# Kernel tuning notes

Measured on AMD Instinct MI355X. Metric: run time of the kernel, lower is better.

The kernel has to match this reference:

```python
import jax, jax.numpy as jnp
import numpy as np
import math

# ---- static configuration (mirrors Renderer defaults) ----
S = 129                                 # density cube side
L = math.ceil(S * math.sqrt(3))         # padded/rotation cube side = 224
C_ABS = 0.2                             # absorption coefficient c
LIGHTS = [
    {'dir': (2, 1, 1),    'rgb': (1.0, 69.0 / 255.0, 25.0 / 255.0)},
    {'dir': (-1, 0.5, 0), 'rgb': (227.0 / 255.0, 1.0, 66.0 / 255.0)},
]


def yp_from_light(l):
    ld = np.asarray(l, dtype=np.float64)
    ld = ld / np.sqrt(np.sum(ld ** 2))
    y = -math.asin(ld[0])
    if ld[2] < 0:
        y = -math.pi - y
    y = y * 180.0 / math.pi
    p = math.asin(ld[1]) * 180.0 / math.pi
    return y, p


def rot_matrix(yaw_deg, pitch_deg, order):
    # yaw about the y (height) axis, pitch about the x axis, roll = 0
    y = math.radians(yaw_deg)
    p = math.radians(pitch_deg)
    Ry = np.array([[math.cos(y), 0.0, math.sin(y)],
                   [0.0, 1.0, 0.0],
                   [-math.sin(y), 0.0, math.cos(y)]], dtype=np.float32)
    Rp = np.array([[1.0, 0.0, 0.0],
                   [0.0, math.cos(p), -math.sin(p)],
                   [0.0, math.sin(p), math.cos(p)]], dtype=np.float32)
    return Ry @ Rp if order == 'ypr' else Rp @ Ry

# base normalized sampling grid (align_corners=True convention), (x,y,z) order
_lin = np.linspace(-1.0, 1.0, L, dtype=np.float32)
_zz, _yy, _xx = np.meshgrid(_lin, _lin, _lin, indexing='ij')
BASE_XYZ = np.stack([_xx, _yy, _zz], axis=-1)   # [L,L,L,3]


def rotate_volume(vol, R):
    """Trilinear resampling of vol [B,C,D,H,W] under rotation R (zero padding)."""
    B, Ch, D, H, W = vol.shape
    src = jnp.einsum('dhwc,kc->dhwk', jnp.asarray(BASE_XYZ), jnp.asarray(R))
    xs = (src[..., 0] + 1.0) * 0.5 * (W - 1)
    ys = (src[..., 1] + 1.0) * 0.5 * (H - 1)
    zs = (src[..., 2] + 1.0) * 0.5 * (D - 1)
    x0 = jnp.floor(xs).astype(jnp.int32)
    y0 = jnp.floor(ys).astype(jnp.int32)
    z0 = jnp.floor(zs).astype(jnp.int32)
    wx = (xs - x0).astype(vol.dtype)
    wy = (ys - y0).astype(vol.dtype)
    wz = (zs - z0).astype(vol.dtype)
    flat = vol.reshape(B, Ch, D * H * W)

    def gather(zi, yi, xi):
        inb = ((zi >= 0) & (zi < D) & (yi >= 0) & (yi < H) & (xi >= 0) & (xi < W)).astype(vol.dtype)
        idx = ((jnp.clip(zi, 0, D - 1) * H + jnp.clip(yi, 0, H - 1)) * W
               + jnp.clip(xi, 0, W - 1)).reshape(-1)
        return jnp.take(flat, idx, axis=2).reshape(B, Ch, D, H, W) * inb

    out = (gather(z0,     y0,     x0)     * ((1 - wz) * (1 - wy) * (1 - wx))
         + gather(z0,     y0,     x0 + 1) * ((1 - wz) * (1 - wy) * wx)
         + gather(z0,     y0 + 1, x0)     * ((1 - wz) * wy * (1 - wx))
         + gather(z0,     y0 + 1, x0 + 1) * ((1 - wz) * wy * wx)
         + gather(z0 + 1, y0,     x0)     * (wz * (1 - wy) * (1 - wx))
         + gather(z0 + 1, y0,     x0 + 1) * (wz * (1 - wy) * wx)
         + gather(z0 + 1, y0 + 1, x0)     * (wz * wy * (1 - wx))
         + gather(z0 + 1, y0 + 1, x0 + 1) * (wz * wy * wx))
    return out


def _revcumsum(a):
    # torch.flip(cumsum(flip(a,[2]),2),[2]) : reverse cumulative sum along depth
    return jnp.flip(jnp.cumsum(jnp.flip(a, 2), axis=2), 2)


def setup_inputs() -> dict:
    key = jax.random.key(0)
    d = jax.random.uniform(key, (1, 1, S, S, S), dtype=jnp.float32)
    return {'d': d}


def reference(d):
    bs, _, Sd, _, _ = d.shape
    i = L // 2 - Sd // 2
    j = i + Sd
    light_array = jnp.zeros((bs, 3, Sd, Sd, Sd), dtype=d.dtype)
    for l in LIGHTS:
        y, p = yp_from_light(l['dir'])
        up = jnp.zeros((bs, 1, L, L, L), dtype=d.dtype).at[:, :, i:j, i:j, i:j].set(d)
        up = rotate_volume(up, rot_matrix(y, p, 'ypr'))
        up = jnp.exp(-C_ABS * _revcumsum(up))           # transmittance toward light
        up = rotate_volume(up, rot_matrix(-y, -p, 'rpy'))
        color = jnp.asarray(l['rgb'], dtype=d.dtype).reshape(1, 3, 1, 1, 1)
        light_array = light_array + up[:, :, i:j, i:j, i:j] * color
    t = jnp.exp(-C_ABS * _revcumsum(d))                  # view-ray transmittance
    out = C_ABS * jnp.sum(d * light_array * t, axis=2)   # background = 0
    return jnp.clip(out, 0.0, 1.0)
```

## Files before the change

### kernel.cpp

```cpp
#include <hip/hip_runtime.h>
#include <hip/hip_fp16.h>
#include <math.h>

#ifndef M_PI
#define M_PI 3.14159265358979323846
#endif

#define SS   129
#define LL   224
#define LL2  (LL*LL)
#define LL3  (LL*LL*LL)
#define SS2  (SS*SS)
#define SS3  (SS*SS*SS)
#define CABS 0.2f
#define PAD  48

#define BLO 45.5f
#define BHI 178.5f

#define NT1  28
#define NTZ16 14
#define ROTG  (2 * NTZ16 * 784)
#define NT3  17
#define NBZ16 9
#define BACKG (2 * NBZ16 * 289)
#define NTZ  28

#define NSEG 16
#define SEGZ 9
#define DSEGT (NSEG * SS2)
#define PREB1 ((DSEGT + 255) / 256)
#define PRERUNB 7
#define N4   (SS3 / 4)
#define CVT4B ((N4 + 1 + 255) / 256)
#define PREG (PREB1 + PRERUNB + CVT4B)
#define SUFG (392 + PREB1)
#define TEXPB (2 * NTZ * LL2 / 256)

#define RBX 21
#define RBY 16
#define RBZ 18
#define RBN (RBX*RBY*RBZ)
#define RSXZ (RBX*RBZ)

#define BBX 21
#define BBY 16
#define BBZ 19
#define BBN (BBX*BBY*BBZ)
#define BSXZ (BBX*BBZ)

struct Mat3 { float m[9]; };
struct F3   { float x, y, z; };

__device__ __forceinline__ F3 tile_center(const Mat3& M, int ox, int oy, int oz) {
    float cbx = fmaf((float)ox + 3.5f, 2.0f / 223.0f, -1.0f);
    float cby = fmaf((float)oy + 3.5f, 2.0f / 223.0f, -1.0f);
    float cbz = fmaf((float)oz + 3.5f, 2.0f / 223.0f, -1.0f);
    F3 qc;
    qc.x = fmaf(fmaf(M.m[0], cbx, fmaf(M.m[1], cby, M.m[2] * cbz)), 111.5f, 111.5f);
    qc.y = fmaf(fmaf(M.m[3], cbx, fmaf(M.m[4], cby, M.m[5] * cbz)), 111.5f, 111.5f);
    qc.z = fmaf(fmaf(M.m[6], cbx, fmaf(M.m[7], cby, M.m[8] * cbz)), 111.5f, 111.5f);
    return qc;
}

__device__ __forceinline__ F3 tile_center16(const Mat3& M, int ox, int oy, int oz) {
    float cbx = fmaf((float)ox + 3.5f, 2.0f / 223.0f, -1.0f);
    float cby = fmaf((float)oy + 3.5f, 2.0f / 223.0f, -1.0f);
    float cbz = fmaf((float)oz + 7.5f, 2.0f / 223.0f, -1.0f);
    F3 qc;
    qc.x = fmaf(fmaf(M.m[0], cbx, fmaf(M.m[1], cby, M.m[2] * cbz)), 111.5f, 111.5f);
    qc.y = fmaf(fmaf(M.m[3], cbx, fmaf(M.m[4], cby, M.m[5] * cbz)), 111.5f, 111.5f);
    qc.z = fmaf(fmaf(M.m[6], cbx, fmaf(M.m[7], cby, M.m[8] * cbz)), 111.5f, 111.5f);
    return qc;
}

__device__ __forceinline__ bool tile_accept(F3 qc, F3 H) {
    return !(qc.x + H.x < BLO || qc.x - H.x > BHI ||
             qc.y + H.y < BLO || qc.y - H.y > BHI ||
             qc.z + H.z < BLO || qc.z - H.z > BHI);
}

__device__ __forceinline__ void qmap(const Mat3& M, int x, int y, int z,
                                     float& qx, float& qy, float& qz) {
    float bx = fmaf((float)x, 2.0f / 223.0f, -1.0f);
    float by = fmaf((float)y, 2.0f / 223.0f, -1.0f);
    float bz = fmaf((float)z, 2.0f / 223.0f, -1.0f);
    qx = fmaf(fmaf(M.m[0], bx, fmaf(M.m[1], by, M.m[2] * bz)), 111.5f, 111.5f);
    qy = fmaf(fmaf(M.m[3], bx, fmaf(M.m[4], by, M.m[5] * bz)), 111.5f, 111.5f);
    qz = fmaf(fmaf(M.m[6], bx, fmaf(M.m[7], by, M.m[8] * bz)), 111.5f, 111.5f);
}

__device__ __forceinline__ float fetch_d(const float* __restrict__ d, int z, int y, int x) {
    unsigned zz = (unsigned)(z - PAD), yy = (unsigned)(y - PAD), xx = (unsigned)(x - PAD);
    return (zz < (unsigned)SS && yy < (unsigned)SS && xx < (unsigned)SS)
        ? d[((int)zz * SS + (int)yy) * SS + (int)xx] : 0.0f;
}

__device__ __forceinline__ float fetch_d16(const __half* __restrict__ d, int z, int y, int x) {
    unsigned zz = (unsigned)(z - PAD), yy = (unsigned)(y - PAD), xx = (unsigned)(x - PAD);
    return (zz < (unsigned)SS && yy < (unsigned)SS && xx < (unsigned)SS)
        ? __half2float(d[((int)zz * SS + (int)yy) * SS + (int)xx]) : 0.0f;
}

__device__ __forceinline__ float fetch_T(const float* __restrict__ T, int z, int y, int x) {
    unsigned zz = (unsigned)z, yy = (unsigned)y, xx = (unsigned)x;
    return (zz < (unsigned)LL && yy < (unsigned)LL && xx < (unsigned)LL)
        ? T[((int)zz * LL + (int)yy) * LL + (int)xx] : 0.0f;
}

__device__ __forceinline__ float tri_T(const float* __restrict__ T, float qz, float qy, float qx) {
    int x0 = (int)floorf(qx), y0 = (int)floorf(qy), z0 = (int)floorf(qz);
    float wx = qx - (float)x0, wy = qy - (float)y0, wz = qz - (float)z0;
    float c000 = fetch_T(T, z0, y0, x0),     c001 = fetch_T(T, z0, y0, x0 + 1);
    float c010 = fetch_T(T, z0, y0 + 1, x0), c011 = fetch_T(T, z0, y0 + 1, x0 + 1);
    float c100 = fetch_T(T, z0 + 1, y0, x0),     c101 = fetch_T(T, z0 + 1, y0, x0 + 1);
    float c110 = fetch_T(T, z0 + 1, y0 + 1, x0), c111 = fetch_T(T, z0 + 1, y0 + 1, x0 + 1);
    float a00 = c000 + wx * (c001 - c000), a01 = c010 + wx * (c011 - c010);
    float a10 = c100 + wx * (c101 - c100), a11 = c110 + wx * (c111 - c110);
    float b0 = a00 + wy * (a01 - a00), b1 = a10 + wy * (a11 - a10);
    return b0 + wz * (b1 - b0);
}

__device__ __forceinline__ float tri_d_g(const float* __restrict__ d, float qz, float qy, float qx) {
    int x0 = (int)floorf(qx), y0 = (int)floorf(qy), z0 = (int)floorf(qz);
    float wx = qx - (float)x0, wy = qy - (float)y0, wz = qz - (float)z0;
    float c000 = fetch_d(d, z0, y0, x0),     c001 = fetch_d(d, z0, y0, x0 + 1);
    float c010 = fetch_d(d, z0, y0 + 1, x0), c011 = fetch_d(d, z0, y0 + 1, x0 + 1);
    float c100 = fetch_d(d, z0 + 1, y0, x0),     c101 = fetch_d(d, z0 + 1, y0, x0 + 1);
    float c110 = fetch_d(d, z0 + 1, y0 + 1, x0), c111 = fetch_d(d, z0 + 1, y0 + 1, x0 + 1);
    float a00 = c000 + wx * (c001 - c000), a01 = c010 + wx * (c011 - c010);
    float a10 = c100 + wx * (c101 - c100), a11 = c110 + wx * (c111 - c110);
    float b0 = a00 + wy * (a01 - a00), b1 = a10 + wy * (a11 - a10);
    return b0 + wz * (b1 - b0);
}

__device__ __forceinline__ float tri_rot(const float* __restrict__ S,
                                         float qx, float qy, float qz,
                                         int lox, int loy, int loz) {
    int x0 = (int)floorf(qx), y0 = (int)floorf(qy), z0 = (int)floorf(qz);
    float wx = qx - (float)x0, wy = qy - (float)y0, wz = qz - (float)z0;
    int i = (y0 - loy) * 378 + (z0 - loz) * 21 + (x0 - lox);
    float c000 = S[i],        c001 = S[i + 1];
    float cz0  = S[i + 21],   cz1  = S[i + 22];
    float cy0  = S[i + 378],  cy1  = S[i + 379];
    float cw0  = S[i + 399],  cw1  = S[i + 400];
    float a00 = c000 + wx * (c001 - c000);
    float a01 = cy0  + wx * (cy1  - cy0);
    float a10 = cz0  + wx * (cz1  - cz0);
    float a11 = cw0  + wx * (cw1  - cw0);
    float b0  = a00 + wy * (a01 - a00);
    float b1  = a10 + wy * (a11 - a10);
    return b0 + wz * (b1 - b0);
}

__device__ __forceinline__ float tri_back(const float* __restrict__ S,
                                          float qx, float qy, float qz,
                                          int lox, int loy, int loz) {
    int x0 = (int)floorf(qx), y0 = (int)floorf(qy), z0 = (int)floorf(qz);
    float wx = qx - (float)x0, wy = qy - (float)y0, wz = qz - (float)z0;
    int i = (y0 - loy) * 399 + (z0 - loz) * 21 + (x0 - lox);
    float c000 = S[i],        c001 = S[i + 1];
    float cz0  = S[i + 21],   cz1  = S[i + 22];
    float cy0  = S[i + 399],  cy1  = S[i + 400];
    float cw0  = S[i + 420],  cw1  = S[i + 421];
    float a00 = c000 + wx * (c001 - c000);
    float a01 = cy0  + wx * (cy1  - cy0);
    float a10 = cz0  + wx * (cz1  - cz0);
    float a11 = cw0  + wx * (cw1  - cw0);
    float b0  = a00 + wy * (a01 - a00);
    float b1  = a10 + wy * (a11 - a10);
    return b0 + wz * (b1 - b0);
}

__global__ __launch_bounds__(256) void k_pre(const float* __restrict__ d,
        float* __restrict__ Dseg, float* __restrict__ A,
        unsigned short* __restrict__ Run, __half* __restrict__ d16,
        Mat3 M0, Mat3 M1, F3 H0, F3 H1) {
    int b = blockIdx.x;
    if (b < PREB1) {
        int t = b * 256 + threadIdx.x;
        if (t < 2 * SS2) A[t] = 0.0f;
        if (t >= DSEGT) return;
        int seg = t / SS2, col = t - seg * SS2;
        int zs = seg * SEGZ, ze = min(SS, zs + SEGZ);
        float run = 0.0f;
        for (int z = zs; z < ze; ++z) run += d[z * SS2 + col];
        Dseg[t] = run;
    } else if (b < PREB1 + PRERUNB) {
        int id = (b - PREB1) * 256 + threadIdx.x;
        if (id >= 2 * 784) return;
        int l = id / 784, r = id - l * 784;
        int ty = r / 28, tx = r - ty * 28;
        const Mat3 M = l ? M1 : M0;
        const F3  H  = l ? H1 : H0;
        int t0 = -1, t1 = -1;
        for (int tz = 0; tz < NT1; ++tz) {
            F3 qc = tile_center(M, tx * 8, ty * 8, tz * 8);
            if (tile_accept(qc, H)) { if (t0 < 0) t0 = tz; t1 = tz; }
        }
        Run[id] = (t0 < 0) ? 0xFFFFu : (unsigned short)(t0 | (t1 << 8));
    } else {
        int t4 = (b - PREB1 - PRERUNB) * 256 + threadIdx.x;
        if (t4 < N4) {
            float4 v = ((const float4*)d)[t4];
            __half2* o = (__half2*)(d16 + 4 * t4);
            o[0] = __floats2half2_rn(v.x, v.y);
            o[1] = __floats2half2_rn(v.z, v.w);
        } else if (t4 == N4) {
            d16[SS3 - 1] = __float2half(d[SS3 - 1]);
        }
    }
}

__global__ __launch_bounds__(512) void k_rot(const __half* __restrict__ d16,
        __half* __restrict__ T0, __half* __restrict__ T1,
        float* __restrict__ S0, float* __restrict__ S1,
        const unsigned short* __restrict__ Run,
        Mat3 M0, Mat3 M1, F3 H0, F3 H1) {
    int b = blockIdx.x;
    int light = b / (NTZ16 * 784);
    int r = b - light * (NTZ16 * 784);
    int tz16 = r / 784;
    int r2 = r - tz16 * 784;
    int tty = r2 / 28, ttx = r2 - tty * 28;

    unsigned short rt = Run[light * 784 + tty * 28 + ttx];
    if (rt == 0xFFFFu) return;
    int t0 = rt & 0xFF, t1 = rt >> 8;
    if (2 * tz16 + 1 < t0 || 2 * tz16 > t1) return;

    const Mat3 M = light ? M1 : M0;
    const F3  H  = light ? H1 : H0;
    __half* __restrict__ T   = light ? T1 : T0;
    float* __restrict__ Ssum = light ? S1 : S0;

    int ox = ttx * 8, oy = tty * 8, oz = tz16 * 16;
    F3 qc = tile_center16(M, ox, oy, oz);

    int lox = (int)floorf(qc.x - H.x);
    int loy = (int)floorf(qc.y - H.y);
    int loz = (int)floorf(qc.z - H.z);

    __shared__ float S[RBN];
    __shared__ float Sc[1024];
    int tid = threadIdx.x;

    if (tid < RSXZ) {
        int ix = tid % RBX, iz = tid / RBX;
        bool interior = (lox >= PAD) & (lox <= PAD + SS - RBX) &
                        (loy >= PAD) & (loy <= PAD + SS - RBY) &
                        (loz >= PAD) & (loz <= PAD + SS - RBZ);
        if (interior) {
            const __half* g = d16 + ((size_t)(loz + iz - PAD) * SS + (loy - PAD)) * SS
                                  + (lox + ix - PAD);
            #pragma unroll
            for (int j = 0; j < RBY; ++j)
                S[tid + j * RSXZ] = __half2float(g[j * SS]);
        } else {
            #pragma unroll
            for (int j = 0; j < RBY; ++j)
                S[tid + j * RSXZ] = fetch_d16(d16, loz + iz, loy + j, lox + ix);
        }
    }
    __syncthreads();

    int lx = tid & 7, ly = (tid >> 3) & 7, lz = tid >> 6;
    int col = tid & 63;
    float fx = (float)lx - 3.5f, fy = (float)ly - 3.5f, fz = (float)lz - 7.5f;
    float qx = qc.x + fmaf(M.m[0], fx, fmaf(M.m[1], fy, M.m[2] * fz));
    float qy = qc.y + fmaf(M.m[3], fx, fmaf(M.m[4], fy, M.m[5] * fz));
    float qz = qc.z + fmaf(M.m[6], fx, fmaf(M.m[7], fy, M.m[8] * fz));
    float v0 = tri_rot(S, qx, qy, qz, lox, loy, loz);
    float qx2 = qx + 8.0f * M.m[2];
    float qy2 = qy + 8.0f * M.m[5];
    float qz2 = qz + 8.0f * M.m[8];
    float v1 = tri_rot(S, qx2, qy2, qz2, lox, loy, loz);

    Sc[lz * 64 + col] = v0;
    Sc[(lz + 8) * 64 + col] = v1;
    __syncthreads();
    if (tid < 128) {
        int c = tid & 63;
        int so = (oy + (c >> 3)) * LL + (ox + (c & 7));
        if (tid < 64) {
            float s = 0.0f;
            #pragma unroll
            for (int k = 15; k >= 8; --k) { s += Sc[k * 64 + c]; Sc[k * 64 + c] = s; }
            Ssum[(2 * tz16 + 1) * LL2 + so] = s;
        } else {
            float s2 = 0.0f;
            #pragma unroll
            for (int k = 7; k >= 0; --k) { s2 += Sc[k * 64 + c]; Sc[k * 64 + c] = s2; }
            Ssum[(2 * tz16) * LL2 + so] = s2;
        }
    }
    __syncthreads();
    int to = (oy + ly) * LL + (ox + lx);
    T[(size_t)(oz + lz) * LL2 + to]     = __float2half(Sc[lz * 64 + col]);
    T[(size_t)(oz + 8 + lz) * LL2 + to] = __float2half(Sc[(lz + 8) * 64 + col]);
}

__global__ __launch_bounds__(256) void k_sufw(float* __restrict__ S0,
        float* __restrict__ S1, const unsigned short* __restrict__ Run,
        const float* __restrict__ d, const float* __restrict__ Dseg,
        __half* __restrict__ W) {
    int b = blockIdx.x;
    if (b < 392) {
        int l = b / 196;
        int col = (b - l * 196) * 256 + threadIdx.x;
        float* __restrict__ Ssum = l ? S1 : S0;
        int x = col % LL, y = col / LL;
        unsigned short r = Run[l * 784 + (y >> 3) * 28 + (x >> 3)];
        if (r == 0xFFFFu) return;
        int t0 = r & 0xFF, t1 = r >> 8;
        float vbuf[NTZ];
        #pragma unroll
        for (int t = 0; t < NTZ; ++t)
            vbuf[t] = (t >= t0 && t <= t1) ? Ssum[t * LL2 + col] : 0.0f;
        float run = 0.0f;
        #pragma unroll
        for (int t = NTZ - 1; t >= 0; --t) {
            if (t >= t0 && t <= t1) Ssum[t * LL2 + col] = run;
            run += vbuf[t];
        }
    } else {
        int t = (b - 392) * 256 + threadIdx.x;
        if (t >= DSEGT) return;
        int seg = t / SS2, col = t - seg * SS2;
        int zs = seg * SEGZ, ze = min(SS, zs + SEGZ);
        float run = 0.0f;
        for (int s2 = seg + 1; s2 < NSEG; ++s2) run += Dseg[s2 * SS2 + col];
        for (int z = ze - 1; z >= zs; --z) {
            float dv = d[z * SS2 + col];
            run += dv;
            W[z * SS2 + col] = __float2half(dv * __expf(-CABS * run));
        }
    }
}

__global__ __launch_bounds__(256) void k_texp(__half* __restrict__ T0,
        __half* __restrict__ T1, const float* __restrict__ S0,
        const float* __restrict__ S1, const unsigned short* __restrict__ Run) {
    int id = blockIdx.x * 256 + threadIdx.x;
    int light = id / (NTZ * LL2);
    int r = id - light * (NTZ * LL2);
    int t = r / LL2, col = r - t * LL2;
    int y = col / LL, x = col - y * LL;
    unsigned short rt = Run[light * 784 + (y >> 3) * 28 + (x >> 3)];
    if (rt == 0xFFFFu) return;
    int t0 = rt & 0xFF, t1 = rt >> 8;
    if (t < t0 || t > t1) return;
    const float* __restrict__ Ssum = light ? S1 : S0;
    __half* __restrict__ T = light ? T1 : T0;
    float off = Ssum[t * LL2 + col];
    size_t base = (size_t)(8 * t) * LL2 + col;
    #pragma unroll
    for (int k = 0; k < 8; ++k) {
        size_t idx = base + (size_t)k * LL2;
        T[idx] = __float2half(__expf(-CABS * (__half2float(T[idx]) + off)));
    }
}

template<bool BINT>
__global__ __launch_bounds__(512) void k_back(const __half* __restrict__ T0,
        const __half* __restrict__ T1, const __half* __restrict__ W,
        float* __restrict__ A0, float* __restrict__ A1,
        Mat3 M0, Mat3 M1, F3 H0, F3 H1) {
    int b = blockIdx.x;
    int light = b / (NBZ16 * 289); b -= light * (NBZ16 * 289);
    int tz16 = b / 289;
    int r2 = b - tz16 * 289;
    int tty = r2 / 17, ttx = r2 - tty * 17;

    const Mat3 M = light ? M1 : M0;
    const F3  H  = light ? H1 : H0;
    const __half* __restrict__ T = light ? T1 : T0;
    float* __restrict__ A = light ? A1 : A0;

    int ox = ttx * 8, oy = tty * 8, oz = tz16 * 16;
    F3 qc = tile_center16(M, ox + PAD, oy + PAD, oz + PAD);
    int lox = (int)floorf(qc.x - H.x);
    int loy = (int)floorf(qc.y - H.y);
    int loz = (int)floorf(qc.z - H.z);

    __shared__ float S[BBN];
    __shared__ float Sc[512];
    int tid = threadIdx.x;

    if (tid < BSXZ) {
        int ix = tid % BBX, iz = tid / BBX;
        if (BINT) {
            const __half* tb = T + ((size_t)(loz + iz) * LL + loy) * LL + (lox + ix);
            #pragma unroll
            for (int j = 0; j < BBY; ++j)
                S[tid + j * BSXZ] = __half2float(tb[j * LL]);
        } else {
            #pragma unroll
            for (int j = 0; j < BBY; ++j) {
                int gz = loz + iz, gy = loy + j, gx = lox + ix;
                bool inb = ((unsigned)gz < (unsigned)LL) & ((unsigned)gy < (unsigned)LL)
                         & ((unsigned)gx < (unsigned)LL);
                S[tid + j * BSXZ] = inb
                    ? __half2float(T[((size_t)gz * LL + gy) * LL + gx]) : 0.0f;
            }
        }
    }
    __syncthreads();

    int lx = tid & 7, ly = (tid >> 3) & 7, lz = tid >> 6;
    int col = tid & 63;
    int x = ox + lx, y = oy + ly;
    float v0 = 0.0f, v1 = 0.0f;
    if (x < SS && y < SS) {
        float fx = (float)lx - 3.5f, fy = (float)ly - 3.5f, fz = (float)lz - 7.5f;
        float qx = qc.x + fmaf(M.m[0], fx, fmaf(M.m[1], fy, M.m[2] * fz));
        float qy = qc.y + fmaf(M.m[3], fx, fmaf(M.m[4], fy, M.m[5] * fz));
        float qz = qc.z + fmaf(M.m[6], fx, fmaf(M.m[7], fy, M.m[8] * fz));
        int z0 = oz + lz, z1 = oz + 8 + lz;
        if (z0 < SS)
            v0 = tri_back(S, qx, qy, qz, lox, loy, loz)
               * __half2float(W[(z0 * SS + y) * SS + x]);
        if (z1 < SS) {
            float qx2 = qx + 8.0f * M.m[2];
            float qy2 = qy + 8.0f * M.m[5];
            float qz2 = qz + 8.0f * M.m[8];
            v1 = tri_back(S, qx2, qy2, qz2, lox, loy, loz)
               * __half2float(W[(z1 * SS + y) * SS + x]);
        }
    }
    Sc[lz * 64 + col] = v0 + v1;
    __syncthreads();
    if (tid < 64) {
        float s = 0.0f;
        #pragma unroll
        for (int k = 0; k < 8; ++k) s += Sc[k * 64 + tid];
        int xx = ox + (tid & 7), yy = oy + (tid >> 3);
        if (xx < SS && yy < SS) atomicAdd(&A[yy * SS + xx], s);
    }
}

__global__ __launch_bounds__(256) void k_combine(const float* __restrict__ A0,
        const float* __restrict__ A1, float* __restrict__ out, F3 c0, F3 c1) {
    int i = blockIdx.x * 256 + threadIdx.x;
    if (i >= 3 * SS2) return;
    int ch = i / SS2, col = i - ch * SS2;
    float r0 = (ch == 0) ? c0.x : ((ch == 1) ? c0.y : c0.z);
    float r1 = (ch == 0) ? c1.x : ((ch == 1) ? c1.y : c1.z);
    float o = CABS * (A0[col] * r0 + A1[col] * r1);
    out[i] = fminf(fmaxf(o, 0.0f), 1.0f);
}

__global__ __launch_bounds__(256) void k_rot_full(const float* __restrict__ d,
                                                  float* __restrict__ T, Mat3 R) {
    int i = blockIdx.x * 256 + threadIdx.x;
    if (i >= LL3) return;
    int x = i % LL; int r = i / LL; int y = r % LL; int z = r / LL;
    float qx, qy, qz; qmap(R, x, y, z, qx, qy, qz);
    T[i] = tri_d_g(d, qz, qy, qx);
}

__global__ __launch_bounds__(256) void k_scan_full(float* __restrict__ T) {
    int col = blockIdx.x * 256 + threadIdx.x;
    if (col >= LL2) return;
    float run = 0.0f;
    for (int z = LL - 1; z >= 0; --z) {
        int idx = z * LL2 + col;
        run += T[idx];
        T[idx] = __expf(-CABS * run);
    }
}

__global__ __launch_bounds__(64) void k_fused_back(const float* __restrict__ T,
        const float* __restrict__ d, float* __restrict__ LA, Mat3 RT,
        float cr, float cg, float cb, int first) {
    int col = blockIdx.x * 64 + threadIdx.x;
    if (col >= SS2) return;
    int y = col / SS, x = col % SS;
    float run = 0.0f, acc = 0.0f;
    for (int z = SS - 1; z >= 0; --z) {
        float qx, qy, qz; qmap(RT, x + PAD, y + PAD, z + PAD, qx, qy, qz);
        float u = tri_T(T, qz, qy, qx);
        float dv = d[z * SS2 + col];
        run += dv;
        acc = fmaf(dv * __expf(-CABS * run), u, acc);
    }
    if (first) {
        LA[0 * SS2 + col] = acc * cr;
        LA[1 * SS2 + col] = acc * cg;
        LA[2 * SS2 + col] = acc * cb;
    } else {
        LA[0 * SS2 + col] += acc * cr;
        LA[1 * SS2 + col] += acc * cg;
        LA[2 * SS2 + col] += acc * cb;
    }
}

__global__ __launch_bounds__(256) void k_clip(const float* __restrict__ LA,
                                              float* __restrict__ out) {
    int i = blockIdx.x * 256 + threadIdx.x;
    if (i < 3 * SS2) out[i] = fminf(fmaxf(CABS * LA[i], 0.0f), 1.0f);
}

static void light_mats(const double ld_in[3], Mat3& R, Mat3& RT) {
    double n = sqrt(ld_in[0]*ld_in[0] + ld_in[1]*ld_in[1] + ld_in[2]*ld_in[2]);
    double l0 = ld_in[0]/n, l1 = ld_in[1]/n, l2 = ld_in[2]/n;
    double yv = -asin(l0);
    if (l2 < 0) yv = -M_PI - yv;
    double yd = yv * 180.0 / M_PI, pd = asin(l1) * 180.0 / M_PI;
    double yr = yd * M_PI / 180.0, pr = pd * M_PI / 180.0;
    float cy = (float)cos(yr), sy = (float)sin(yr), cp = (float)cos(pr), sp = (float)sin(pr);
    float m[9] = { cy,  sy*sp,  sy*cp,
                   0.f, cp,    -sp,
                  -sy,  cy*sp,  cy*cp };
    for (int i = 0; i < 9; ++i) R.m[i] = m[i];
    RT.m[0] = m[0]; RT.m[1] = m[3]; RT.m[2] = m[6];
    RT.m[3] = m[1]; RT.m[4] = m[4]; RT.m[5] = m[7];
    RT.m[6] = m[2]; RT.m[7] = m[5]; RT.m[8] = m[8];
}

static F3 half_span8(const Mat3& M) {
    F3 h;
    h.x = 3.5f * (fabsf(M.m[0]) + fabsf(M.m[1]) + fabsf(M.m[2])) + 0.05f;
    h.y = 3.5f * (fabsf(M.m[3]) + fabsf(M.m[4]) + fabsf(M.m[5])) + 0.05f;
    h.z = 3.5f * (fabsf(M.m[6]) + fabsf(M.m[7]) + fabsf(M.m[8])) + 0.05f;
    return h;
}

static F3 half_span16(const Mat3& M) {
    F3 h;
    h.x = 3.5f * (fabsf(M.m[0]) + fabsf(M.m[1])) + 7.5f * fabsf(M.m[2]) + 0.1f;
    h.y = 3.5f * (fabsf(M.m[3]) + fabsf(M.m[4])) + 7.5f * fabsf(M.m[5]) + 0.1f;
    h.z = 3.5f * (fabsf(M.m[6]) + fabsf(M.m[7])) + 7.5f * fabsf(M.m[8]) + 0.1f;
    return h;
}

static void h_qc16(const Mat3& M, double ox, double oy, double oz, double q[3]) {
    double cb[3] = { (ox + 3.5) * 2.0 / 223.0 - 1.0,
                     (oy + 3.5) * 2.0 / 223.0 - 1.0,
                     (oz + 7.5) * 2.0 / 223.0 - 1.0 };
    for (int k = 0; k < 3; ++k)
        q[k] = ((double)M.m[3*k] * cb[0] + (double)M.m[3*k+1] * cb[1]
              + (double)M.m[3*k+2] * cb[2]) * 111.5 + 111.5;
}

extern "C" void kernel_launch(void* const* d_in, const int* in_sizes, int n_in,
                              void* d_out, int out_size, void* d_ws, size_t ws_size,
                              hipStream_t stream) {
    const float* d = (const float*)d_in[0];
    float* out = (float*)d_out;

    const double dirs[2][3] = { {2.0, 1.0, 1.0}, {-1.0, 0.5, 0.0} };
    F3 c0 = { 1.0f, 69.0f / 255.0f, 25.0f / 255.0f };
    F3 c1 = { 227.0f / 255.0f, 1.0f, 66.0f / 255.0f };
    Mat3 R[2], RT[2];
    light_mats(dirs[0], R[0], RT[0]);
    light_mats(dirs[1], R[1], RT[1]);
    F3 H8[2]  = { half_span8(R[0]),  half_span8(R[1])  };
    F3 H16[2] = { half_span16(R[0]), half_span16(R[1]) };
    F3 HB[2]  = { half_span16(RT[0]), half_span16(RT[1]) };

    bool bint = true;
    for (int l = 0; l < 2 && bint; ++l) {
        double H[3] = { HB[l].x, HB[l].y, HB[l].z };
        int dim[3] = { BBX, BBY, BBZ };
        for (int tz = 0; tz < NBZ16 && bint; ++tz)
            for (int ty = 0; ty < NT3 && bint; ++ty)
                for (int tx = 0; tx < NT3; ++tx) {
                    double q[3]; h_qc16(RT[l], tx * 8 + PAD, ty * 8 + PAD, tz * 16 + PAD, q);
                    for (int k = 0; k < 3; ++k) {
                        int lo = (int)floor(q[k] - H[k]);
                        if (lo < 1 || lo + dim[k] > LL - 1) { bint = false; break; }
                    }
                    if (!bint) break;
                }
    }

    const size_t f32n = (size_t)(2 * NTZ * LL2 + NSEG * SS2 + 2 * SS2);
    const size_t need_A = f32n * 4 + (size_t)(SS3 + 2 * LL3) * 2 + 2 * 784 * 2;
    const size_t need_C = (size_t)(LL3 + 3 * SS2) * 4;

    if (ws_size >= need_A) {
        float* S0   = (float*)d_ws;
        float* S1   = S0 + NTZ * LL2;
        float* Dseg = S1 + NTZ * LL2;
        float* A0   = Dseg + NSEG * SS2;
        float* A1   = A0 + SS2;
        __half* d16 = (__half*)(A1 + SS2);
        __half* W   = d16;
        __half* T0  = d16 + SS3;
        __half* T1  = T0 + LL3;
        unsigned short* Run = (unsigned short*)(T1 + LL3);

        k_pre  <<<PREG, 256, 0, stream>>>(d, Dseg, A0, Run, d16,
                                          R[0], R[1], H8[0], H8[1]);
        k_rot  <<<ROTG, 512, 0, stream>>>(d16, T0, T1, S0, S1, Run,
                                          R[0], R[1], H16[0], H16[1]);
        k_sufw <<<SUFG, 256, 0, stream>>>(S0, S1, Run, d, Dseg, W);
        k_texp <<<TEXPB, 256, 0, stream>>>(T0, T1, S0, S1, Run);
        if (bint)
            k_back<true><<<BACKG, 512, 0, stream>>>(T0, T1, W, A0, A1,
                                                    RT[0], RT[1], HB[0], HB[1]);
        else
            k_back<false><<<BACKG, 512, 0, stream>>>(T0, T1, W, A0, A1,
                                                     RT[0], RT[1], HB[0], HB[1]);
        k_combine<<<(3 * SS2 + 255) / 256, 256, 0, stream>>>(A0, A1, out, c0, c1);
    } else if (ws_size >= need_C) {
        float* T  = (float*)d_ws;
        float* LA = T + LL3;
        for (int l = 0; l < 2; ++l) {
            k_rot_full <<<(LL3 + 255) / 256, 256, 0, stream>>>(d, T, R[l]);
            k_scan_full<<<(LL2 + 255) / 256, 256, 0, stream>>>(T);
            k_fused_back<<<(SS2 + 63) / 64, 64, 0, stream>>>(T, d, LA, RT[l],
                l ? c1.x : c0.x, l ? c1.y : c0.y, l ? c1.z : c0.z, l == 0);
        }
        k_clip<<<(3 * SS2 + 255) / 256, 256, 0, stream>>>(LA, out);
    }
}
```

Measured before the change: 174.0 us.

## Remap block IDs across XCDs and vectorize half-precision loads/stores in rot/back kernels

Block indices in k_rot and k_back are remapped so that each group of 8 consecutive hardware blocks, which round-robin across the MI355X's XCDs, maps to contiguous chunks of spatially adjacent tiles. The goal is better per-XCD L2 locality. k_rot now writes its fp16 output as 16-byte vector stores from 128 threads, replacing scalar half stores. k_back aligns the tile x-origin to even and widens the shared tile to 22 columns so it can load __half2 pairs. The cost is padded grid blocks that exit early and a slightly larger shared tile, and the host-side bounds check is updated to match the alignment.

```diff
diff --git a/kernel.cpp b/kernel.cpp
--- a/kernel.cpp
+++ b/kernel.cpp
@@ -21,9 +21,12 @@
 #define NT1  28
 #define NTZ16 14
 #define ROTG  (2 * NTZ16 * 784)
+#define ROTCH 392
 #define NT3  17
 #define NBZ16 9
 #define BACKG (2 * NBZ16 * 289)
+#define BACKCH 17
+#define BACKG_P 5304
 #define NTZ  28
 
 #define NSEG 16
@@ -43,11 +46,12 @@
 #define RBN (RBX*RBY*RBZ)
 #define RSXZ (RBX*RBZ)
 
-#define BBX 21
+#define BBX 22
 #define BBY 16
 #define BBZ 19
+#define BBXZ (BBX*BBZ)
 #define BBN (BBX*BBY*BBZ)
-#define BSXZ (BBX*BBZ)
+#define BSXZ2 (11*BBZ)
 
 struct Mat3 { float m[9]; };
 struct F3   { float x, y, z; };
@@ -158,11 +162,11 @@
                                           int lox, int loy, int loz) {
     int x0 = (int)floorf(qx), y0 = (int)floorf(qy), z0 = (int)floorf(qz);
     float wx = qx - (float)x0, wy = qy - (float)y0, wz = qz - (float)z0;
-    int i = (y0 - loy) * 399 + (z0 - loz) * 21 + (x0 - lox);
+    int i = (y0 - loy) * BBXZ + (z0 - loz) * BBX + (x0 - lox);
     float c000 = S[i],        c001 = S[i + 1];
-    float cz0  = S[i + 21],   cz1  = S[i + 22];
-    float cy0  = S[i + 399],  cy1  = S[i + 400];
-    float cw0  = S[i + 420],  cw1  = S[i + 421];
+    float cz0  = S[i + 22],   cz1  = S[i + 23];
+    float cy0  = S[i + 418],  cy1  = S[i + 419];
+    float cw0  = S[i + 440],  cw1  = S[i + 441];
     float a00 = c000 + wx * (c001 - c000);
     float a01 = cy0  + wx * (cy1  - cy0);
     float a10 = cz0  + wx * (cz1  - cz0);
@@ -217,7 +221,11 @@
         float* __restrict__ S0, float* __restrict__ S1,
         const unsigned short* __restrict__ Run,
         Mat3 M0, Mat3 M1, F3 H0, F3 H1) {
-    int b = blockIdx.x;
+    int n = blockIdx.x;
+    int x8 = n & 7, i8 = n >> 3;
+    int c = i8 / ROTCH, off = i8 - c * ROTCH;
+    int b = (c * 8 + x8) * ROTCH + off;
+
     int light = b / (NTZ16 * 784);
     int r = b - light * (NTZ16 * 784);
     int tz16 = r / 784;
@@ -280,24 +288,33 @@
     Sc[(lz + 8) * 64 + col] = v1;
     __syncthreads();
     if (tid < 128) {
-        int c = tid & 63;
-        int so = (oy + (c >> 3)) * LL + (ox + (c & 7));
+        int cc = tid & 63;
+        int so = (oy + (cc >> 3)) * LL + (ox + (cc & 7));
         if (tid < 64) {
             float s = 0.0f;
             #pragma unroll
-            for (int k = 15; k >= 8; --k) { s += Sc[k * 64 + c]; Sc[k * 64 + c] = s; }
+            for (int k = 15; k >= 8; --k) { s += Sc[k * 64 + cc]; Sc[k * 64 + cc] = s; }
             Ssum[(2 * tz16 + 1) * LL2 + so] = s;
         } else {
             float s2 = 0.0f;
             #pragma unroll
-            for (int k = 7; k >= 0; --k) { s2 += Sc[k * 64 + c]; Sc[k * 64 + c] = s2; }
+            for (int k = 7; k >= 0; --k) { s2 += Sc[k * 64 + cc]; Sc[k * 64 + cc] = s2; }
             Ssum[(2 * tz16) * LL2 + so] = s2;
         }
     }
     __syncthreads();
-    int to = (oy + ly) * LL + (ox + lx);
-    T[(size_t)(oz + lz) * LL2 + to]     = __float2half(Sc[lz * 64 + col]);
-    T[(size_t)(oz + 8 + lz) * LL2 + to] = __float2half(Sc[(lz + 8) * 64 + col]);
+    if (tid < 128) {
+        int zz = tid >> 3, ly2 = tid & 7;
+        const float4* Sc4 = (const float4*)Sc;
+        float4 f0 = Sc4[zz * 16 + ly2 * 2];
+        float4 f1 = Sc4[zz * 16 + ly2 * 2 + 1];
+        union { __half2 h[4]; float4 v; } u;
+        u.h[0] = __floats2half2_rn(f0.x, f0.y);
+        u.h[1] = __floats2half2_rn(f0.z, f0.w);
+        u.h[2] = __floats2half2_rn(f1.x, f1.y);
+        u.h[3] = __floats2half2_rn(f1.z, f1.w);
+        *(float4*)&T[(size_t)(oz + zz) * LL2 + (oy + ly2) * LL + ox] = u.v;
+    }
 }
 
 __global__ __launch_bounds__(256) void k_sufw(float* __restrict__ S0,
@@ -366,10 +383,15 @@
         const __half* __restrict__ T1, const __half* __restrict__ W,
         float* __restrict__ A0, float* __restrict__ A1,
         Mat3 M0, Mat3 M1, F3 H0, F3 H1) {
-    int b = blockIdx.x;
-    int light = b / (NBZ16 * 289); b -= light * (NBZ16 * 289);
-    int tz16 = b / 289;
-    int r2 = b - tz16 * 289;
+    int n = blockIdx.x;
+    int x8 = n & 7, i8 = n >> 3;
+    int c = i8 / BACKCH, off = i8 - c * BACKCH;
+    int lb = (c * 8 + x8) * BACKCH + off;
+    if (lb >= BACKG) return;
+
+    int light = lb / (NBZ16 * 289); lb -= light * (NBZ16 * 289);
+    int tz16 = lb / 289;
+    int r2 = lb - tz16 * 289;
     int tty = r2 / 17, ttx = r2 - tty * 17;
 
     const Mat3 M = light ? M1 : M0;
@@ -380,6 +402,7 @@
     int ox = ttx * 8, oy = tty * 8, oz = tz16 * 16;
     F3 qc = tile_center16(M, ox + PAD, oy + PAD, oz + PAD);
     int lox = (int)floorf(qc.x - H.x);
+    lox &= ~1;
     int loy = (int)floorf(qc.y - H.y);
     int loz = (int)floorf(qc.z - H.z);
 
@@ -387,21 +410,30 @@
     __shared__ float Sc[512];
     int tid = threadIdx.x;
 
-    if (tid < BSXZ) {
-        int ix = tid % BBX, iz = tid / BBX;
+    if (tid < BSXZ2) {
+        int ixh = tid % 11, iz = tid / 11;
         if (BINT) {
-            const __half* tb = T + ((size_t)(loz + iz) * LL + loy) * LL + (lox + ix);
-            #pragma unroll
-            for (int j = 0; j < BBY; ++j)
-                S[tid + j * BSXZ] = __half2float(tb[j * LL]);
-        } else {
+            const __half2* tb = (const __half2*)
+                (T + ((size_t)(loz + iz) * LL + loy) * LL + lox);
             #pragma unroll
             for (int j = 0; j < BBY; ++j) {
-                int gz = loz + iz, gy = loy + j, gx = lox + ix;
-                bool inb = ((unsigned)gz < (unsigned)LL) & ((unsigned)gy < (unsigned)LL)
-                         & ((unsigned)gx < (unsigned)LL);
-                S[tid + j * BSXZ] = inb
-                    ? __half2float(T[((size_t)gz * LL + gy) * LL + gx]) : 0.0f;
+                float2 f = __half22float2(tb[j * (LL / 2) + ixh]);
+                int si = j * BBXZ + iz * BBX + 2 * ixh;
+                *(float2*)&S[si] = f;
+            }
+        } else {
+            int gx0 = lox + 2 * ixh, gx1 = gx0 + 1;
+            #pragma unroll
+            for (int j = 0; j < BBY; ++j) {
+                int gz = loz + iz, gy = loy + j;
+                bool zy = ((unsigned)gz < (unsigned)LL) & ((unsigned)gy < (unsigned)LL);
+                size_t rowb = ((size_t)gz * LL + gy) * LL;
+                float e0 = (zy && (unsigned)gx0 < (unsigned)LL)
+                         ? __half2float(T[rowb + gx0]) : 0.0f;
+                float e1 = (zy && (unsigned)gx1 < (unsigned)LL)
+                         ? __half2float(T[rowb + gx1]) : 0.0f;
+                int si = j * BBXZ + iz * BBX + 2 * ixh;
+                S[si] = e0; S[si + 1] = e1;
             }
         }
     }
@@ -569,6 +601,7 @@
                     double q[3]; h_qc16(RT[l], tx * 8 + PAD, ty * 8 + PAD, tz * 16 + PAD, q);
                     for (int k = 0; k < 3; ++k) {
                         int lo = (int)floor(q[k] - H[k]);
+                        if (k == 0) lo &= ~1;
                         if (lo < 1 || lo + dim[k] > LL - 1) { bint = false; break; }
                     }
                     if (!bint) break;
@@ -598,11 +631,11 @@
         k_sufw <<<SUFG, 256, 0, stream>>>(S0, S1, Run, d, Dseg, W);
         k_texp <<<TEXPB, 256, 0, stream>>>(T0, T1, S0, S1, Run);
         if (bint)
-            k_back<true><<<BACKG, 512, 0, stream>>>(T0, T1, W, A0, A1,
-                                                    RT[0], RT[1], HB[0], HB[1]);
+            k_back<true><<<BACKG_P, 512, 0, stream>>>(T0, T1, W, A0, A1,
+                                                      RT[0], RT[1], HB[0], HB[1]);
         else
-            k_back<false><<<BACKG, 512, 0, stream>>>(T0, T1, W, A0, A1,
-                                                     RT[0], RT[1], HB[0], HB[1]);
+            k_back<false><<<BACKG_P, 512, 0, stream>>>(T0, T1, W, A0, A1,
+                                                       RT[0], RT[1], HB[0], HB[1]);
         k_combine<<<(3 * SS2 + 255) / 256, 256, 0, stream>>>(A0, A1, out, c0, c1);
     } else if (ws_size >= need_C) {
         float* T  = (float*)d_ws;
```

Result: slower. 185.3 us (+6.5%).
